# Kernel optimization log

Hardware: AMD Instinct MI355X
Metric: run time of the kernel (lower is better)

The kernel has to match this reference:

```python
import jax, jax.numpy as jnp
import numpy as np

DN = jax.lax.conv_dimension_numbers((1, 32, 32, 32, 1), (3, 3, 3, 1, 32), ('NDHWC', 'DHWIO', 'NDHWC'))


def setup_inputs() -> dict:
    key = jax.random.key(0)
    k0, k1, k2, k3, k4 = jax.random.split(key, 5)
    B = 64
    x = jax.random.normal(k0, (B, 32, 32, 32, 1), dtype=jnp.float32)
    # conv weights in DHWIO layout; kaiming-ish scale
    w1 = jax.random.normal(k1, (3, 3, 3, 1, 32), dtype=jnp.float32) * (1.0 / np.sqrt(27 * 1))
    b1 = jax.random.normal(k2, (32,), dtype=jnp.float32) * 0.01
    w2 = jax.random.normal(k3, (3, 3, 3, 32, 64), dtype=jnp.float32) * (1.0 / np.sqrt(27 * 32))
    b2 = jax.random.normal(k4, (64,), dtype=jnp.float32) * 0.01
    return {"x": x, "w1": w1, "b1": b1, "w2": w2, "b2": b2}


def _conv3d_valid(x, w):
    # x: [B, D, H, W, C_in], w: [kD, kH, kW, C_in, C_out] -> [B, D-2, H-2, W-2, C_out]
    dn = jax.lax.conv_dimension_numbers(x.shape, w.shape, ('NDHWC', 'DHWIO', 'NDHWC'))
    return jax.lax.conv_general_dilated(x, w, window_strides=(1, 1, 1),
                                        padding='VALID', dimension_numbers=dn)


def reference(x, w1, b1, w2, b2):
    # Dense input -> all voxels active, so spconv's gather-GEMM-scatter equals
    # a dense valid 3D conv. ReLU acts on active-site features == dense ReLU.
    h = jax.nn.relu(_conv3d_valid(x, w1) + b1)        # [B, 30, 30, 30, 32]
    h = jax.nn.relu(_conv3d_valid(h, w2) + b2)        # [B, 28, 28, 28, 64]
    # spconv ToDense returns NCDHW
    return jnp.transpose(h, (0, 4, 1, 2, 3))          # [B, 64, 28, 28, 28]
```

## Files before the change

### kernel.cpp

```cpp
#include <hip/hip_runtime.h>
#include <cstdint>
#include <cstddef>

typedef __attribute__((ext_vector_type(8))) short bf16x8;
typedef __attribute__((ext_vector_type(4))) float f32x4;
typedef __attribute__((ext_vector_type(4))) unsigned int u32x4;
typedef unsigned short u16;

#define H1_ROW_B   1920
#define H1_BATCH   (30 * 30 * 960)
#define LDS_STRIDE 1952
#define OUT_CSTR   21952

__device__ __forceinline__ u16 f2bf(float f) {
    union { float f; unsigned u; } v; v.f = f;
    unsigned r = v.u + 0x7FFF + ((v.u >> 16) & 1);
    return (u16)(r >> 16);
}

__device__ __forceinline__ void fma4(float4& a, float s, const float4& w) {
    a.x = fmaf(s, w.x, a.x);
    a.y = fmaf(s, w.y, a.y);
    a.z = fmaf(s, w.z, a.z);
    a.w = fmaf(s, w.w, a.w);
}

__device__ __forceinline__ void gld_lds(const char* src, unsigned char* dst) {
    __builtin_amdgcn_global_load_lds(
        (const __attribute__((address_space(1))) void*)src,
        (__attribute__((address_space(3))) void*)dst, 16, 0, 0);
}

__global__ __launch_bounds__(256) void conv1_relu(
    const float* __restrict__ x, const float* __restrict__ w1,
    const float* __restrict__ b1, u16* __restrict__ h1, int b0)
{
    __shared__ float xs[3 * 8 * 32];

    const int z   = blockIdx.x;
    const int yt  = blockIdx.y;
    const int bl  = blockIdx.z;
    const int b   = b0 + bl;
    const int tid = threadIdx.x;
    const int y0  = yt * 6;

    if (tid < 192) {
        const int idx = tid * 4;
        const int zp  = idx >> 8;
        const int rem = idx & 255;
        const int yy  = rem >> 5;
        const int xx  = rem & 31;
        const float4 v = *reinterpret_cast<const float4*>(
            x + (size_t)b * 32768 + ((size_t)(z + zp) * 32 + (y0 + yy)) * 32 + xx);
        *reinterpret_cast<float4*>(&xs[idx]) = v;
    }

    const int c4   = tid & 7;
    const int slot = tid >> 3;

    float4 wr[27];
#pragma unroll
    for (int t = 0; t < 27; ++t)
        wr[t] = *reinterpret_cast<const float4*>(w1 + t * 32 + c4 * 4);
    const float4 bias = *reinterpret_cast<const float4*>(b1 + c4 * 4);

    __syncthreads();

    u16* h1b = h1 + (size_t)bl * H1_BATCH;

    if (slot < 30) {
#pragma unroll
        for (int j = 0; j < 3; ++j) {
            const int p  = slot + 30 * j;
            const int yy = p / 15;
            const int xx = (p - yy * 15) * 2;
            const int y  = y0 + yy;

            float4 acc0 = bias, acc1 = bias;
#pragma unroll
            for (int kd = 0; kd < 3; ++kd) {
#pragma unroll
                for (int kh = 0; kh < 3; ++kh) {
                    const float* row = &xs[((kd * 8) + (yy + kh)) * 32 + xx];
                    const float2 v01 = *reinterpret_cast<const float2*>(row);
                    const float2 v23 = *reinterpret_cast<const float2*>(row + 2);
                    const int t = (kd * 3 + kh) * 3;
                    fma4(acc0, v01.x, wr[t + 0]);
                    fma4(acc0, v01.y, wr[t + 1]);
                    fma4(acc0, v23.x, wr[t + 2]);
                    fma4(acc1, v01.y, wr[t + 0]);
                    fma4(acc1, v23.x, wr[t + 1]);
                    fma4(acc1, v23.y, wr[t + 2]);
                }
            }
            ushort4 s0, s1;
            s0.x = f2bf(fmaxf(acc0.x, 0.f)); s0.y = f2bf(fmaxf(acc0.y, 0.f));
            s0.z = f2bf(fmaxf(acc0.z, 0.f)); s0.w = f2bf(fmaxf(acc0.w, 0.f));
            s1.x = f2bf(fmaxf(acc1.x, 0.f)); s1.y = f2bf(fmaxf(acc1.y, 0.f));
            s1.z = f2bf(fmaxf(acc1.z, 0.f)); s1.w = f2bf(fmaxf(acc1.w, 0.f));
            u16* dst = h1b + ((size_t)(z * 30 + y) * 30 + xx) * 32 + c4 * 4;
            *reinterpret_cast<ushort4*>(dst)      = s0;
            *reinterpret_cast<ushort4*>(dst + 32) = s1;
        }
    }
}

__global__ __launch_bounds__(256) void pack_w2(
    const float* __restrict__ w2, u16* __restrict__ wB)
{
    const int tap = blockIdx.x;
    const int tid = threadIdx.x;
    const int nt = tid >> 6;
    const int l  = tid & 63;
    const int r = l & 15, q = l >> 4;
    u16* dst = wB + ((size_t)(tap * 4 + nt) * 64 + l) * 8;
#pragma unroll
    for (int j = 0; j < 8; ++j)
        dst[j] = f2bf(w2[(size_t)(tap * 32 + q * 8 + j) * 64 + nt * 16 + r]);
}

__global__ __launch_bounds__(512, 4) void conv2_mfma(
    const u16* __restrict__ h1, const u16* __restrict__ wB,
    const float* __restrict__ b2, float* __restrict__ out, int b0)
{
    __shared__ __align__(16) unsigned char smem[36 * LDS_STRIDE];

    const int g   = gridDim.x;
    const int bid = blockIdx.x;
    const int lb  = (g % 8 == 0) ? ((bid & 7) * (g >> 3) + (bid >> 3)) : bid;

    const int t0  = lb % 49;
    const int bl  = lb / 49;
    const int yg  = t0 % 7;
    const int zt  = t0 / 7;

    const int b  = b0 + bl;
    const int y0 = yg * 4, z0 = zt * 4;
    const int tid = threadIdx.x;
    const int wv  = tid >> 6;
    const int l   = tid & 63;
    const int zw  = wv >> 1;
    const int nh  = wv & 1;
    const int r = l & 15, q = l >> 4;
    const int yl = r >> 2, xg = r & 3;

    const char* wBl = (const char*)wB + nh * 2048 + l * 16;

    {
        const char* gbase = (const char*)(h1 + (size_t)bl * H1_BATCH);
        for (int c = wv; c < 72; c += 8) {
            const int rid = c >> 1, half = c & 1;
            const int zz = rid / 6, yy = rid - zz * 6;
            const char* src = gbase
                + (size_t)((z0 + zz) * 30 + (y0 + yy)) * H1_ROW_B
                + half * 896 + l * 16;
            unsigned char* dst = smem + rid * LDS_STRIDE + half * 896 + l * 16;
            gld_lds(src, dst);
        }
    }
    __syncthreads();

    f32x4 acc[7][2];
    {
        const float bv0 = b2[nh * 32 + r];
        const float bv1 = b2[nh * 32 + 16 + r];
#pragma unroll
        for (int mt = 0; mt < 7; ++mt) {
            acc[mt][0] = (f32x4){bv0, bv0, bv0, bv0};
            acc[mt][1] = (f32x4){bv1, bv1, bv1, bv1};
        }
    }

    const unsigned char* aBase =
        smem + (zw * 6 + yl) * LDS_STRIDE + xg * 64 + q * 16;

    u32x4 Bs[3][2];
#define B_LOAD(slot, t)                                                        \
    { const char* p_ = wBl + (size_t)(t) * 4096;                               \
      asm volatile("global_load_dwordx4 %0, %2, off\n\t"                       \
                   "global_load_dwordx4 %1, %2, off offset:1024"               \
                   : "=&v"(Bs[slot][0]), "=&v"(Bs[slot][1]) : "v"(p_)); }

    B_LOAD(0, 0)
    B_LOAD(1, 1)

#pragma unroll
    for (int tap = 0; tap < 27; ++tap) {
        const int cur = tap % 3;

        if (tap < 25) B_LOAD((tap + 2) % 3, tap + 2)

        if (tap < 25)       asm volatile("s_waitcnt vmcnt(4)");
        else if (tap == 25) asm volatile("s_waitcnt vmcnt(2)");
        else                asm volatile("s_waitcnt vmcnt(0)");

        asm volatile("" : "+v"(Bs[cur][0]), "+v"(Bs[cur][1]));
        const bf16x8 B0 = __builtin_bit_cast(bf16x8, Bs[cur][0]);
        const bf16x8 B1 = __builtin_bit_cast(bf16x8, Bs[cur][1]);

        const int kd = tap / 9;
        const int kh = (tap - kd * 9) / 3;
        const int kw = tap - kd * 9 - kh * 3;
        const unsigned char* ap = aBase + (kd * 6 + kh) * LDS_STRIDE + kw * 64;

#pragma unroll
        for (int mt = 0; mt < 7; ++mt) {
            const bf16x8 a = *reinterpret_cast<const bf16x8*>(ap + mt * 256);
            acc[mt][0] = __builtin_amdgcn_mfma_f32_16x16x32_bf16(a, B0, acc[mt][0], 0, 0, 0);
            acc[mt][1] = __builtin_amdgcn_mfma_f32_16x16x32_bf16(a, B1, acc[mt][1], 0, 0, 0);
        }
    }
#undef B_LOAD

    const int z = z0 + zw;
    float* ob = out + ((size_t)b * 64 + nh * 32 + r) * OUT_CSTR
                    + (size_t)z * 784 + (size_t)(y0 + q) * 28;
#pragma unroll
    for (int mt = 0; mt < 7; ++mt) {
#pragma unroll
        for (int nt = 0; nt < 2; ++nt) {
            const f32x4 v = acc[mt][nt];
            float4 st;
            st.x = fmaxf(v.x, 0.f);
            st.y = fmaxf(v.y, 0.f);
            st.z = fmaxf(v.z, 0.f);
            st.w = fmaxf(v.w, 0.f);
            *reinterpret_cast<float4*>(ob + (size_t)nt * 16 * OUT_CSTR + mt * 4) = st;
        }
    }
}

extern "C" void kernel_launch(void* const* d_in, const int* in_sizes, int n_in,
                              void* d_out, int out_size, void* d_ws, size_t ws_size,
                              hipStream_t stream)
{
    const float* x  = (const float*)d_in[0];
    const float* w1 = (const float*)d_in[1];
    const float* b1 = (const float*)d_in[2];
    const float* w2 = (const float*)d_in[3];
    const float* b2 = (const float*)d_in[4];
    float* out = (float*)d_out;

    u16* wB = (u16*)d_ws;
    u16* h1 = (u16*)((char*)d_ws + 131072);

    pack_w2<<<27, 256, 0, stream>>>(w2, wB);

    const size_t per_batch = (size_t)H1_BATCH * 2;
    size_t avail = ws_size > 131072 ? ws_size - 131072 : 0;
    int bchunk = (int)(avail / per_batch);
    if (bchunk < 1)  bchunk = 1;
    if (bchunk > 64) bchunk = 64;

    for (int b0 = 0; b0 < 64; b0 += bchunk) {
        int bc = 64 - b0;
        if (bc > bchunk) bc = bchunk;
        conv1_relu<<<dim3(30, 5, bc), 256, 0, stream>>>(x, w1, b1, h1, b0);
        conv2_mfma<<<dim3(49 * bc), 512, 0, stream>>>(h1, wB, b2, out, b0);
    }
}
```

Measured before the change: 255.8 us.

## Switch conv2 to 32x32x16 MFMA with swizzled h1 layout and new weight packing

Changes the second convolution from 16x16x32 bf16 MFMA tiles (7 M-tiles x 2 N-tiles per wave) to 32x32x16 MFMA tiles covering both 32-channel output halves per wave. The conv1 output and the packed weights are re-laid out to match: h1 channels are XOR-swizzled within each voxel, and the LDS A-fragment reads apply the same swizzle, which is intended to avoid LDS bank conflicts. Weight prefetch goes from triple-buffered pairs to double-buffered quads of 16-byte loads. The larger MFMA shape is meant to raise math throughput per instruction and cut LDS reads per FLOP. The overlapping x tiles (0-15 and 12-27) recompute some outputs, and the store pattern changes.

```diff
diff --git a/kernel.cpp b/kernel.cpp
--- a/kernel.cpp
+++ b/kernel.cpp
@@ -3,7 +3,7 @@
 #include <cstddef>
 
 typedef __attribute__((ext_vector_type(8))) short bf16x8;
-typedef __attribute__((ext_vector_type(4))) float f32x4;
+typedef __attribute__((ext_vector_type(16))) float f32x16;
 typedef __attribute__((ext_vector_type(4))) unsigned int u32x4;
 typedef unsigned short u16;
 
@@ -73,7 +73,8 @@
         for (int j = 0; j < 3; ++j) {
             const int p  = slot + 30 * j;
             const int yy = p / 15;
-            const int xx = (p - yy * 15) * 2;
+            const int xp = p - yy * 15;
+            const int xx = xp * 2;
             const int y  = y0 + yy;
 
             float4 acc0 = bias, acc1 = bias;
@@ -98,7 +99,9 @@
             s0.z = f2bf(fmaxf(acc0.z, 0.f)); s0.w = f2bf(fmaxf(acc0.w, 0.f));
             s1.x = f2bf(fmaxf(acc1.x, 0.f)); s1.y = f2bf(fmaxf(acc1.y, 0.f));
             s1.z = f2bf(fmaxf(acc1.z, 0.f)); s1.w = f2bf(fmaxf(acc1.w, 0.f));
-            u16* dst = h1b + ((size_t)(z * 30 + y) * 30 + xx) * 32 + c4 * 4;
+            const int s2 = xp & 3;
+            u16* dst = h1b + ((size_t)(z * 30 + y) * 30 + xx) * 32
+                           + ((c4 * 4) ^ (s2 << 3));
             *reinterpret_cast<ushort4*>(dst)      = s0;
             *reinterpret_cast<ushort4*>(dst + 32) = s1;
         }
@@ -110,13 +113,16 @@
 {
     const int tap = blockIdx.x;
     const int tid = threadIdx.x;
-    const int nt = tid >> 6;
+    const int f  = tid >> 6;
     const int l  = tid & 63;
-    const int r = l & 15, q = l >> 4;
-    u16* dst = wB + ((size_t)(tap * 4 + nt) * 64 + l) * 8;
-#pragma unroll
-    for (int j = 0; j < 8; ++j)
-        dst[j] = f2bf(w2[(size_t)(tap * 32 + q * 8 + j) * 64 + nt * 16 + r]);
+    const int ks = f >> 1, nf = f & 1;
+    const int co = nf * 32 + (l & 31);
+    u16* dst = wB + ((size_t)(tap * 4 + f) * 64 + l) * 8;
+#pragma unroll
+    for (int j = 0; j < 8; ++j) {
+        const int ci = ks * 16 + (l >> 5) * 8 + j;
+        dst[j] = f2bf(w2[(size_t)(tap * 32 + ci) * 64 + co]);
+    }
 }
 
 __global__ __launch_bounds__(512, 4) void conv2_mfma(
@@ -140,16 +146,18 @@
     const int wv  = tid >> 6;
     const int l   = tid & 63;
     const int zw  = wv >> 1;
-    const int nh  = wv & 1;
-    const int r = l & 15, q = l >> 4;
-    const int yl = r >> 2, xg = r & 3;
-
-    const char* wBl = (const char*)wB + nh * 2048 + l * 16;
+    const int mh  = wv & 1;
+    const int c   = l & 31;
+    const int kh  = l >> 5;
+    const int xi  = l & 15;
+    const int yl  = (l >> 4) & 1;
+
+    const char* wBl = (const char*)wB + (size_t)l * 16;
 
     {
         const char* gbase = (const char*)(h1 + (size_t)bl * H1_BATCH);
-        for (int c = wv; c < 72; c += 8) {
-            const int rid = c >> 1, half = c & 1;
+        for (int cc = wv; cc < 72; cc += 8) {
+            const int rid = cc >> 1, half = cc & 1;
             const int zz = rid / 6, yy = rid - zz * 6;
             const char* src = gbase
                 + (size_t)((z0 + zz) * 30 + (y0 + yy)) * H1_ROW_B
@@ -160,72 +168,101 @@
     }
     __syncthreads();
 
-    f32x4 acc[7][2];
+    f32x16 acc[2][2];
     {
-        const float bv0 = b2[nh * 32 + r];
-        const float bv1 = b2[nh * 32 + 16 + r];
-#pragma unroll
-        for (int mt = 0; mt < 7; ++mt) {
-            acc[mt][0] = (f32x4){bv0, bv0, bv0, bv0};
-            acc[mt][1] = (f32x4){bv1, bv1, bv1, bv1};
-        }
-    }
-
-    const unsigned char* aBase =
-        smem + (zw * 6 + yl) * LDS_STRIDE + xg * 64 + q * 16;
-
-    u32x4 Bs[3][2];
+        const float bv0 = b2[c];
+        const float bv1 = b2[32 + c];
+#pragma unroll
+        for (int i = 0; i < 16; ++i) {
+            acc[0][0][i] = bv0; acc[1][0][i] = bv0;
+            acc[0][1][i] = bv1; acc[1][1][i] = bv1;
+        }
+    }
+
+    const unsigned char* aRow =
+        smem + (size_t)(mh * 2 + yl) * LDS_STRIDE + (size_t)zw * (6 * LDS_STRIDE);
+    int xoff[2][3], swx[2][3];
+#pragma unroll
+    for (int mt = 0; mt < 2; ++mt)
+#pragma unroll
+        for (int kw = 0; kw < 3; ++kw) {
+            const int xin = mt * 12 + xi + kw;
+            xoff[mt][kw] = xin * 64;
+            swx[mt][kw]  = (xin >> 1) & 3;
+        }
+    const int kc0 = kh, kc1 = 2 + kh;
+
+    u32x4 Bs[2][4];
 #define B_LOAD(slot, t)                                                        \
     { const char* p_ = wBl + (size_t)(t) * 4096;                               \
-      asm volatile("global_load_dwordx4 %0, %2, off\n\t"                       \
-                   "global_load_dwordx4 %1, %2, off offset:1024"               \
-                   : "=&v"(Bs[slot][0]), "=&v"(Bs[slot][1]) : "v"(p_)); }
+      asm volatile("global_load_dwordx4 %0, %4, off\n\t"                       \
+                   "global_load_dwordx4 %1, %4, off offset:1024\n\t"           \
+                   "global_load_dwordx4 %2, %4, off offset:2048\n\t"           \
+                   "global_load_dwordx4 %3, %4, off offset:3072"               \
+                   : "=&v"(Bs[slot][0]), "=&v"(Bs[slot][1]),                   \
+                     "=&v"(Bs[slot][2]), "=&v"(Bs[slot][3])                    \
+                   : "v"(p_)); }
 
     B_LOAD(0, 0)
-    B_LOAD(1, 1)
 
 #pragma unroll
     for (int tap = 0; tap < 27; ++tap) {
-        const int cur = tap % 3;
-
-        if (tap < 25) B_LOAD((tap + 2) % 3, tap + 2)
-
-        if (tap < 25)       asm volatile("s_waitcnt vmcnt(4)");
-        else if (tap == 25) asm volatile("s_waitcnt vmcnt(2)");
-        else                asm volatile("s_waitcnt vmcnt(0)");
-
-        asm volatile("" : "+v"(Bs[cur][0]), "+v"(Bs[cur][1]));
-        const bf16x8 B0 = __builtin_bit_cast(bf16x8, Bs[cur][0]);
-        const bf16x8 B1 = __builtin_bit_cast(bf16x8, Bs[cur][1]);
-
-        const int kd = tap / 9;
-        const int kh = (tap - kd * 9) / 3;
-        const int kw = tap - kd * 9 - kh * 3;
-        const unsigned char* ap = aBase + (kd * 6 + kh) * LDS_STRIDE + kw * 64;
-
-#pragma unroll
-        for (int mt = 0; mt < 7; ++mt) {
-            const bf16x8 a = *reinterpret_cast<const bf16x8*>(ap + mt * 256);
-            acc[mt][0] = __builtin_amdgcn_mfma_f32_16x16x32_bf16(a, B0, acc[mt][0], 0, 0, 0);
-            acc[mt][1] = __builtin_amdgcn_mfma_f32_16x16x32_bf16(a, B1, acc[mt][1], 0, 0, 0);
+        const int cur = tap & 1;
+
+        if (tap < 26) B_LOAD(cur ^ 1, tap + 1)
+
+        if (tap < 26) asm volatile("s_waitcnt vmcnt(4)");
+        else          asm volatile("s_waitcnt vmcnt(0)");
+
+        asm volatile("" : "+v"(Bs[cur][0]), "+v"(Bs[cur][1]),
+                          "+v"(Bs[cur][2]), "+v"(Bs[cur][3]));
+        const bf16x8 B00 = __builtin_bit_cast(bf16x8, Bs[cur][0]);
+        const bf16x8 B01 = __builtin_bit_cast(bf16x8, Bs[cur][1]);
+        const bf16x8 B10 = __builtin_bit_cast(bf16x8, Bs[cur][2]);
+        const bf16x8 B11 = __builtin_bit_cast(bf16x8, Bs[cur][3]);
+
+        const int kd  = tap / 9;
+        const int khp = (tap - kd * 9) / 3;
+        const int kw  = tap - kd * 9 - khp * 3;
+        const unsigned char* rp = aRow + (kd * 6 + khp) * LDS_STRIDE;
+
+#pragma unroll
+        for (int mt = 0; mt < 2; ++mt) {
+            const int xo = xoff[mt][kw];
+            const int sw = swx[mt][kw];
+            const bf16x8 a0 = *reinterpret_cast<const bf16x8*>(
+                rp + xo + ((kc0 ^ sw) << 4));
+            const bf16x8 a1 = *reinterpret_cast<const bf16x8*>(
+                rp + xo + ((kc1 ^ sw) << 4));
+            acc[mt][0] = __builtin_amdgcn_mfma_f32_32x32x16_bf16(a0, B00, acc[mt][0], 0, 0, 0);
+            acc[mt][1] = __builtin_amdgcn_mfma_f32_32x32x16_bf16(a0, B01, acc[mt][1], 0, 0, 0);
+            acc[mt][0] = __builtin_amdgcn_mfma_f32_32x32x16_bf16(a1, B10, acc[mt][0], 0, 0, 0);
+            acc[mt][1] = __builtin_amdgcn_mfma_f32_32x32x16_bf16(a1, B11, acc[mt][1], 0, 0, 0);
         }
     }
 #undef B_LOAD
 
     const int z = z0 + zw;
-    float* ob = out + ((size_t)b * 64 + nh * 32 + r) * OUT_CSTR
-                    + (size_t)z * 784 + (size_t)(y0 + q) * 28;
-#pragma unroll
-    for (int mt = 0; mt < 7; ++mt) {
-#pragma unroll
-        for (int nt = 0; nt < 2; ++nt) {
-            const f32x4 v = acc[mt][nt];
-            float4 st;
-            st.x = fmaxf(v.x, 0.f);
-            st.y = fmaxf(v.y, 0.f);
-            st.z = fmaxf(v.z, 0.f);
-            st.w = fmaxf(v.w, 0.f);
-            *reinterpret_cast<float4*>(ob + (size_t)nt * 16 * OUT_CSTR + mt * 4) = st;
+    const int ybase = y0 + mh * 2;
+#pragma unroll
+    for (int mt = 0; mt < 2; ++mt) {
+        const int x0 = mt * 12;
+#pragma unroll
+        for (int nf = 0; nf < 2; ++nf) {
+            const int co = nf * 32 + c;
+            float* ob = out + ((size_t)b * 64 + co) * OUT_CSTR
+                            + (size_t)z * 784 + (size_t)ybase * 28 + x0;
+#pragma unroll
+            for (int qd = 0; qd < 4; ++qd) {
+                const int yy = qd >> 1;
+                const int xo = (qd & 1) * 8 + 4 * kh;
+                float4 st;
+                st.x = fmaxf(acc[mt][nf][qd * 4 + 0], 0.f);
+                st.y = fmaxf(acc[mt][nf][qd * 4 + 1], 0.f);
+                st.z = fmaxf(acc[mt][nf][qd * 4 + 2], 0.f);
+                st.w = fmaxf(acc[mt][nf][qd * 4 + 3], 0.f);
+                *reinterpret_cast<float4*>(ob + yy * 28 + xo) = st;
+            }
         }
     }
 }
```

After: 279.1 us. 1.09x slower.
